# Kernel optimization log

Measured on AMD Instinct MI355X. Metric: run time of the kernel, lower is better.

Reference implementation:

```python
import jax, jax.numpy as jnp
import numpy as np

N, E, H, C = 20000, 320000, 4, 64
F_NODE, F_EDGE, F_W, T, LH = 64, 16, 8, 24, 64
NEG_SLOPE, EPS = 0.2, 1e-5


def setup_inputs() -> dict:
    key = jax.random.key(0)
    ks = jax.random.split(key, 20)
    d = {
        'node_static_features': jax.random.normal(ks[0], (N, F_NODE), jnp.float32),
        'edge_static_features': jax.random.normal(ks[1], (E, F_EDGE), jnp.float32),
        'node_dynamic_features': jax.random.normal(ks[2], (N, T, F_W), jnp.float32),
        'edge_index': jax.random.randint(ks[3], (E, 2), 0, N, jnp.int64),
        # GATConv params (PyG layout): shared lin for src/dst, lin_edge, att vectors, bias
        'W_lin': jax.random.normal(ks[4], (F_NODE, H * C), jnp.float32) / np.sqrt(F_NODE),
        'W_edge': jax.random.normal(ks[5], (F_EDGE, H * C), jnp.float32) / np.sqrt(F_EDGE),
        'att_src': jax.random.normal(ks[6], (H, C), jnp.float32) / np.sqrt(C),
        'att_dst': jax.random.normal(ks[7], (H, C), jnp.float32) / np.sqrt(C),
        'att_edge': jax.random.normal(ks[8], (H, C), jnp.float32) / np.sqrt(C),
        'gat_bias': jnp.zeros((C,), jnp.float32),
        # BatchNorm
        'bn_gamma': jnp.ones((C,), jnp.float32),
        'bn_beta': jnp.zeros((C,), jnp.float32),
        # LSTM (torch gate order i,f,g,o)
        'W_ih': jax.random.normal(ks[9], (4 * LH, F_W), jnp.float32) / np.sqrt(F_W),
        'W_hh': jax.random.normal(ks[10], (4 * LH, LH), jnp.float32) / np.sqrt(LH),
        'b_ih': jnp.zeros((4 * LH,), jnp.float32),
        'b_hh': jnp.zeros((4 * LH,), jnp.float32),
        # MLP head
        'W_hid': jax.random.normal(ks[11], (C + LH, C // 2), jnp.float32) / np.sqrt(C + LH),
        'b_hid': jnp.zeros((C // 2,), jnp.float32),
        'W_out': jax.random.normal(ks[12], (C // 2, 1), jnp.float32) / np.sqrt(C // 2),
        'b_out': jnp.zeros((1,), jnp.float32),
    }
    return d


def _gat_forward(x, edge_attr, src, dst, W_lin, W_edge, att_src, att_dst, att_edge, gat_bias):
    # add self loops with edge_attr fill_value='mean' (per-target mean of incoming edge feats)
    deg = jax.ops.segment_sum(jnp.ones((src.shape[0],), x.dtype), dst, num_segments=N)
    mean_attr = jax.ops.segment_sum(edge_attr, dst, num_segments=N) / jnp.maximum(deg, 1.0)[:, None]
    loop = jnp.arange(N, dtype=src.dtype)
    src = jnp.concatenate([src, loop]); dst = jnp.concatenate([dst, loop])
    edge_attr = jnp.concatenate([edge_attr, mean_attr], axis=0)  # [E+N, F_EDGE]

    xh = (x @ W_lin).reshape(N, H, C)                              # [N,H,C]
    eh = (edge_attr @ W_edge).reshape(-1, H, C)                    # [E+N,H,C]
    a_src = jnp.einsum('nhc,hc->nh', xh, att_src)                  # [N,H]
    a_dst = jnp.einsum('nhc,hc->nh', xh, att_dst)
    a_edge = jnp.einsum('ehc,hc->eh', eh, att_edge)
    alpha = a_src[src] + a_dst[dst] + a_edge                       # [E+N,H]
    alpha = jax.nn.leaky_relu(alpha, NEG_SLOPE)
    # segment softmax over edges grouped by destination node
    amax = jax.ops.segment_max(alpha, dst, num_segments=N)
    amax = jnp.where(jnp.isfinite(amax), amax, 0.0)
    ex = jnp.exp(alpha - amax[dst])
    denom = jax.ops.segment_sum(ex, dst, num_segments=N)
    attn = ex / (denom[dst] + 1e-16)                               # [E+N,H]
    msg = xh[src] * attn[:, :, None]                               # [E+N,H,C]
    out = jax.ops.segment_sum(msg, dst, num_segments=N)            # [N,H,C]
    return out.mean(axis=1) + gat_bias                             # concat=False -> head mean


def _lstm_last(xs, W_ih, W_hh, b_ih, b_hh):
    # xs: [N, T, F_W]; returns h_T: [N, LH]
    def step(carry, x_t):
        h, c = carry
        g = x_t @ W_ih.T + b_ih + h @ W_hh.T + b_hh
        i, f, gg, o = jnp.split(g, 4, axis=-1)
        c = jax.nn.sigmoid(f) * c + jax.nn.sigmoid(i) * jnp.tanh(gg)
        h = jax.nn.sigmoid(o) * jnp.tanh(c)
        return (h, c), None
    h0 = jnp.zeros((xs.shape[0], LH), xs.dtype)
    (h, _), _ = jax.lax.scan(step, (h0, h0), jnp.swapaxes(xs, 0, 1))
    return h


def reference(node_static_features, edge_static_features, node_dynamic_features, edge_index,
              W_lin, W_edge, att_src, att_dst, att_edge, gat_bias,
              bn_gamma, bn_beta, W_ih, W_hh, b_ih, b_hh,
              W_hid, b_hid, W_out, b_out):
    src, dst = edge_index[:, 0], edge_index[:, 1]
    x1 = _gat_forward(node_static_features, edge_static_features, src, dst,
                      W_lin, W_edge, att_src, att_dst, att_edge, gat_bias)
    # BatchNorm1d (training-mode batch stats) + relu; dropout is identity at eval
    mu = x1.mean(axis=0)
    var = x1.var(axis=0)
    x1 = jax.nn.relu((x1 - mu) / jnp.sqrt(var + EPS) * bn_gamma + bn_beta)
    h_last = _lstm_last(node_dynamic_features, W_ih, W_hh, b_ih, b_hh)  # [N,LH]
    combined = jnp.concatenate([x1, h_last], axis=1)
    hidden = jax.nn.relu(combined @ W_hid + b_hid)
    return hidden @ W_out + b_out  # [N,1]
```

## Files before the change

### kernel.cpp

```cpp
#include <hip/hip_runtime.h>
#include <hip/hip_bf16.h>

constexpr int N_  = 20000;
constexpr int E_  = 320000;
constexpr int T_  = 24;
constexpr float NEG_ = 0.2f;
constexpr float EPS_ = 1e-5f;
constexpr int MAXD_ = 128;
constexpr int LNB_ = 8;

typedef __attribute__((ext_vector_type(8)))  short short8v;
typedef __attribute__((ext_vector_type(16))) float f32x16;

__device__ __forceinline__ int esrc(const int* __restrict__ p, int e, int f64) {
    return f64 ? p[4 * e] : p[2 * e];
}
__device__ __forceinline__ int edst(const int* __restrict__ p, int e, int f64) {
    return f64 ? p[4 * e + 2] : p[2 * e + 1];
}

__device__ __forceinline__ float sigf(float x) {
    return __builtin_amdgcn_rcpf(1.f + __expf(-x));
}
__device__ __forceinline__ float tanhfast(float x) {
    return 1.f - 2.f * __builtin_amdgcn_rcpf(1.f + __expf(2.f * x));
}

__device__ __forceinline__ short f2bf(float f) {
    union { float f; unsigned u; } v; v.f = f;
    unsigned r = v.u + 0x7FFFu + ((v.u >> 16) & 1u);
    return (short)(r >> 16);
}
__device__ __forceinline__ float bf2f(unsigned short u) {
    return __uint_as_float((unsigned)u << 16);
}

__global__ void k_detect(const int* __restrict__ idx, int* __restrict__ flag) {
    int v = idx[2 * threadIdx.x + 1];
    unsigned long long b = __ballot(v != 0);
    if (threadIdx.x == 0) flag[0] = (b == 0ULL) ? 1 : 0;
}

__global__ __launch_bounds__(256) void k_Pq(
    const float* __restrict__ W_edge, const float* __restrict__ att_edge,
    const float* __restrict__ att_src, const float* __restrict__ att_dst,
    const float* __restrict__ W_lin, float* __restrict__ P, float* __restrict__ Q) {
    int t = threadIdx.x;
    if (t < 64) {
        int k = t >> 2, h = t & 3;
        float s = 0.f;
        for (int c = 0; c < 64; ++c) s += W_edge[k * 256 + h * 64 + c] * att_edge[h * 64 + c];
        P[k * 4 + h] = s;
    }
    {
        int k = t >> 2, h = t & 3;
        float s = 0.f, d = 0.f;
        for (int c = 0; c < 64; ++c) {
            float w = W_lin[k * 256 + h * 64 + c];
            s += w * att_src[h * 64 + c];
            d += w * att_dst[h * 64 + c];
        }
        Q[k * 8 + h] = s;
        Q[k * 8 + 4 + h] = d;
    }
}

__global__ __launch_bounds__(256) void k_node(
    const float* __restrict__ x, const float* __restrict__ W_lin,
    const float* __restrict__ Q,
    unsigned short* __restrict__ xhb, float* __restrict__ asrc, float* __restrict__ adst) {
    __shared__ float xs[16][65];
    __shared__ float Qsh[64][8];
    int t = threadIdx.x;
    int nb = blockIdx.x * 16;
    for (int i = t; i < 16 * 64; i += 256) xs[i >> 6][i & 63] = x[(long)nb * 64 + i];
    for (int i = t; i < 64 * 8; i += 256) ((float*)Qsh)[i] = Q[i];
    __syncthreads();
    float acc[16];
#pragma unroll
    for (int m = 0; m < 16; ++m) acc[m] = 0.f;
    for (int k = 0; k < 64; ++k) {
        float w = W_lin[k * 256 + t];
#pragma unroll
        for (int m = 0; m < 16; ++m) acc[m] += xs[m][k] * w;
    }
#pragma unroll
    for (int m = 0; m < 16; ++m) xhb[(long)(nb + m) * 256 + t] = (unsigned short)f2bf(acc[m]);
    if (t < 128) {
        int m = t >> 3, q = t & 7;
        float s = 0.f;
        for (int k = 0; k < 64; ++k) s += xs[m][k] * Qsh[k][q];
        if (q < 4) asrc[(nb + m) * 4 + q] = s;
        else       adst[(nb + m) * 4 + (q - 4)] = s;
    }
}

__global__ __launch_bounds__(256) void k_e1(
    const int* __restrict__ idx, const int* __restrict__ flag,
    const float* __restrict__ ea, const float* __restrict__ P,
    float4* __restrict__ aebuf, int* __restrict__ degi) {
    __shared__ float Ps[256];
    int t = threadIdx.x;
    if (t < 64) Ps[t] = P[t];
    __syncthreads();
    int e = blockIdx.x * 256 + t;
    if (e >= E_) return;
    int f64 = flag[0];
    int d = edst(idx, e, f64);
    const float* ep = ea + (long)e * 16;
    float ae[4] = {0.f, 0.f, 0.f, 0.f};
#pragma unroll
    for (int k = 0; k < 16; ++k) {
        float v = ep[k];
#pragma unroll
        for (int h = 0; h < 4; ++h) ae[h] += v * Ps[k * 4 + h];
    }
    aebuf[e] = make_float4(ae[0], ae[1], ae[2], ae[3]);
    atomicAdd(&degi[d], 1);
}

__global__ __launch_bounds__(256) void k_scan(const int* __restrict__ degi,
                                              int* __restrict__ offs) {
    __shared__ int part[256];
    int t = threadIdx.x;
    int base = t * 80;
    int s = 0;
    for (int i = 0; i < 80; ++i) { int ix = base + i; if (ix < N_) s += degi[ix]; }
    part[t] = s;
    __syncthreads();
    for (int d = 1; d < 256; d <<= 1) {
        int v = (t >= d) ? part[t - d] : 0;
        __syncthreads();
        part[t] += v;
        __syncthreads();
    }
    int run = (t > 0) ? part[t - 1] : 0;
    for (int i = 0; i < 80; ++i) {
        int ix = base + i;
        if (ix < N_) { offs[ix] = run; run += degi[ix]; }
    }
}

__global__ __launch_bounds__(256) void k_e2(
    const int* __restrict__ idx, const int* __restrict__ flag,
    const int* __restrict__ offs, int* __restrict__ cursor,
    int2* __restrict__ csr) {
    int e = blockIdx.x * 256 + threadIdx.x;
    if (e >= E_) return;
    int f64 = flag[0];
    int d = edst(idx, e, f64);
    int s = esrc(idx, e, f64);
    int pos = atomicAdd(&cursor[d], 1);
    csr[offs[d] + pos] = make_int2(e, s);
}

__global__ __launch_bounds__(256) void k_n2(
    const int* __restrict__ offs, const int* __restrict__ degi,
    const int2* __restrict__ csr, const float4* __restrict__ aebuf,
    const float4* __restrict__ asrc4, const float4* __restrict__ adst4,
    const unsigned short* __restrict__ xhb, const float* __restrict__ gat_bias,
    float* __restrict__ x1) {
    __shared__ int   sS[4][MAXD_];
    __shared__ float4 sEx[4][MAXD_];
    int t = threadIdx.x, w = t >> 6, lane = t & 63;
    int n = blockIdx.x * 4 + w;
    if (n >= N_) return;
    int deg = degi[n], off = offs[n];
    float4 ad = adst4[n];

    float4 aesum = make_float4(0, 0, 0, 0), den = make_float4(0, 0, 0, 0);
    for (int base = 0; base < deg; base += 64) {
        int i = base + lane;
        if (i < deg) {
            int2 pr = csr[off + i];
            float4 ae = aebuf[pr.x];
            float4 as = asrc4[pr.y];
            float a0 = as.x + ad.x + ae.x; a0 = a0 > 0.f ? a0 : NEG_ * a0;
            float a1 = as.y + ad.y + ae.y; a1 = a1 > 0.f ? a1 : NEG_ * a1;
            float a2 = as.z + ad.z + ae.z; a2 = a2 > 0.f ? a2 : NEG_ * a2;
            float a3 = as.w + ad.w + ae.w; a3 = a3 > 0.f ? a3 : NEG_ * a3;
            float4 ex = make_float4(__expf(a0), __expf(a1), __expf(a2), __expf(a3));
            aesum.x += ae.x; aesum.y += ae.y; aesum.z += ae.z; aesum.w += ae.w;
            den.x += ex.x; den.y += ex.y; den.z += ex.z; den.w += ex.w;
            if (i < MAXD_) { sS[w][i] = pr.y; sEx[w][i] = ex; }
        }
    }
#pragma unroll
    for (int m = 32; m >= 1; m >>= 1) {
        aesum.x += __shfl_xor(aesum.x, m); aesum.y += __shfl_xor(aesum.y, m);
        aesum.z += __shfl_xor(aesum.z, m); aesum.w += __shfl_xor(aesum.w, m);
        den.x += __shfl_xor(den.x, m); den.y += __shfl_xor(den.y, m);
        den.z += __shfl_xor(den.z, m); den.w += __shfl_xor(den.w, m);
    }
    float dv = fmaxf((float)deg, 1.f);
    float4 as = asrc4[n];
    float a0 = as.x + ad.x + aesum.x / dv; a0 = a0 > 0.f ? a0 : NEG_ * a0;
    float a1 = as.y + ad.y + aesum.y / dv; a1 = a1 > 0.f ? a1 : NEG_ * a1;
    float a2 = as.z + ad.z + aesum.z / dv; a2 = a2 > 0.f ? a2 : NEG_ * a2;
    float a3 = as.w + ad.w + aesum.w / dv; a3 = a3 > 0.f ? a3 : NEG_ * a3;
    float4 exs = make_float4(__expf(a0), __expf(a1), __expf(a2), __expf(a3));
    den.x += exs.x; den.y += exs.y; den.z += exs.z; den.w += exs.w;
    float i0 = 1.f / (den.x + 1e-16f), i1 = 1.f / (den.y + 1e-16f);
    float i2 = 1.f / (den.z + 1e-16f), i3 = 1.f / (den.w + 1e-16f);
    __syncthreads();

    float acc = 0.f;
#pragma unroll 2
    for (int i = 0; i < deg; ++i) {
        int s; float4 ex;
        if (i < MAXD_) { s = sS[w][i]; ex = sEx[w][i]; }
        else {
            int2 pr = csr[off + i];
            s = pr.y;
            float4 ae = aebuf[pr.x];
            float4 a5 = asrc4[s];
            float b0 = a5.x + ad.x + ae.x; b0 = b0 > 0.f ? b0 : NEG_ * b0;
            float b1 = a5.y + ad.y + ae.y; b1 = b1 > 0.f ? b1 : NEG_ * b1;
            float b2 = a5.z + ad.z + ae.z; b2 = b2 > 0.f ? b2 : NEG_ * b2;
            float b3 = a5.w + ad.w + ae.w; b3 = b3 > 0.f ? b3 : NEG_ * b3;
            ex = make_float4(__expf(b0), __expf(b1), __expf(b2), __expf(b3));
        }
        const unsigned short* xp = xhb + (long)s * 256;
        acc += ex.x * i0 * bf2f(xp[lane]) + ex.y * i1 * bf2f(xp[64 + lane])
             + ex.z * i2 * bf2f(xp[128 + lane]) + ex.w * i3 * bf2f(xp[192 + lane]);
    }
    {
        const unsigned short* xp = xhb + (long)n * 256;
        acc += exs.x * i0 * bf2f(xp[lane]) + exs.y * i1 * bf2f(xp[64 + lane])
             + exs.z * i2 * bf2f(xp[128 + lane]) + exs.w * i3 * bf2f(xp[192 + lane]);
    }
    x1[(long)n * 64 + lane] = acc * 0.25f + gat_bias[lane];
}

__global__ __launch_bounds__(256) void k_x1stats(
    const float* __restrict__ x1, float* __restrict__ bnsum) {
    int c = threadIdx.x & 63, r = threadIdx.x >> 6;
    float s = 0.f, s2 = 0.f;
    for (int n = blockIdx.x * 4 + r; n < N_; n += gridDim.x * 4) {
        float v = x1[(long)n * 64 + c];
        s += v; s2 += v * v;
    }
    __shared__ float red[4][128];
    red[r][c] = s; red[r][64 + c] = s2;
    __syncthreads();
    if (r == 0) {
        float ts = red[0][c] + red[1][c] + red[2][c] + red[3][c];
        float t2 = red[0][64 + c] + red[1][64 + c] + red[2][64 + c] + red[3][64 + c];
        atomicAdd(&bnsum[c], ts);
        atomicAdd(&bnsum[64 + c], t2);
    }
}

__global__ void k_bnfin(const float* __restrict__ bnsum, const float* __restrict__ gamma,
                        const float* __restrict__ beta, float* __restrict__ bnp) {
    int c = threadIdx.x;
    float mu = bnsum[c] / (float)N_;
    float var = bnsum[64 + c] / (float)N_ - mu * mu;
    float sc = gamma[c] * rsqrtf(var + EPS_);
    bnp[c] = sc;
    bnp[64 + c] = beta[c] - mu * sc;
}

__global__ __launch_bounds__(256, 2) void k_lstm_mfma(
    const float* __restrict__ xdyn, const float* __restrict__ W_ih,
    const float* __restrict__ W_hh, const float* __restrict__ b_ih,
    const float* __restrict__ b_hh, float* __restrict__ hlast) {
    __shared__ char lds[57344];
    char* W2b = lds + 32768;
    int t = threadIdx.x;
    int w = t >> 6, l = t & 63;
    int lm = l & 31, g = l >> 5;

    for (int idx = t; idx < 2048; idx += 256) {
        int ll = idx & 63, ks = (idx >> 6) & 3, t8 = idx >> 8;
        int j = 32 * t8 + (ll & 31);
        const float* wp = W_hh + j * 64 + 16 * ks + 8 * (ll >> 5);
        float4 wa = *(const float4*)wp;
        float4 wb = *(const float4*)(wp + 4);
        short8v f;
        f[0] = f2bf(wa.x); f[1] = f2bf(wa.y); f[2] = f2bf(wa.z); f[3] = f2bf(wa.w);
        f[4] = f2bf(wb.x); f[5] = f2bf(wb.y); f[6] = f2bf(wb.z); f[7] = f2bf(wb.w);
        *(short8v*)(lds + idx * 16) = f;
    }
    for (int idx = t; idx < 512; idx += 256) {
        int ll = idx & 63, t8 = idx >> 6;
        int j = 32 * t8 + (ll & 31);
        short8v f;
        if (ll < 32) {
            const float* wp = W_ih + j * 8;
            float4 wa = *(const float4*)wp;
            float4 wb = *(const float4*)(wp + 4);
            f[0] = f2bf(wa.x); f[1] = f2bf(wa.y); f[2] = f2bf(wa.z); f[3] = f2bf(wa.w);
            f[4] = f2bf(wb.x); f[5] = f2bf(wb.y); f[6] = f2bf(wb.z); f[7] = f2bf(wb.w);
        } else {
#pragma unroll
            for (int e = 0; e < 8; ++e) f[e] = 0;
            f[0] = f2bf(b_ih[j] + b_hh[j]);
        }
        *(short8v*)(W2b + idx * 16) = f;
    }
    char* Hb = lds + 40960 + w * 4096;
    {
        short8v zv;
#pragma unroll
        for (int e = 0; e < 8; ++e) zv[e] = 0;
#pragma unroll
        for (int i = l; i < 256; i += 64) ((short8v*)Hb)[i] = zv;
    }
    __syncthreads();

    const int nbase = blockIdx.x * 32 + w * LNB_;
    f32x16 zc;
#pragma unroll
    for (int e = 0; e < 16; ++e) zc[e] = 0.f;
    short8v xAc;
#pragma unroll
    for (int e = 0; e < 8; ++e) xAc[e] = 0;
    xAc[0] = (short)0x3F80;
    float cst[2][4];
#pragma unroll
    for (int jt = 0; jt < 2; ++jt)
#pragma unroll
        for (int r = 0; r < 4; ++r) cst[jt][r] = 0.f;

    const bool xld = (g == 0) && (lm < LNB_);
    const float* xbase = xdyn + (long)(nbase + (lm & (LNB_ - 1))) * T_ * 8;
    float4 xp0 = make_float4(0, 0, 0, 0), xp1 = make_float4(0, 0, 0, 0);
    if (xld) { xp0 = *(const float4*)xbase; xp1 = *(const float4*)(xbase + 4); }

    for (int t_ = 0; t_ < T_; ++t_) {
        short8v xA;
        if (g == 0) {
            if (xld) {
                xA[0] = f2bf(xp0.x); xA[1] = f2bf(xp0.y); xA[2] = f2bf(xp0.z); xA[3] = f2bf(xp0.w);
                xA[4] = f2bf(xp1.x); xA[5] = f2bf(xp1.y); xA[6] = f2bf(xp1.z); xA[7] = f2bf(xp1.w);
                if (t_ < T_ - 1) {
                    xp0 = *(const float4*)(xbase + (t_ + 1) * 8);
                    xp1 = *(const float4*)(xbase + (t_ + 1) * 8 + 4);
                }
            } else {
#pragma unroll
                for (int e = 0; e < 8; ++e) xA[e] = 0;
            }
        } else xA = xAc;

        short8v hA[4];
#pragma unroll
        for (int ks = 0; ks < 4; ++ks) {
            int raddr = (lm * 128 + 32 * ks + 16 * g) ^ ((lm & 7) << 4);
            hA[ks] = *(const short8v*)(Hb + raddr);
        }

        f32x16 acc[8];
#pragma unroll
        for (int t8 = 0; t8 < 8; ++t8) {
            short8v b2f = *(const short8v*)(W2b + (t8 * 64 + l) * 16);
            acc[t8] = __builtin_amdgcn_mfma_f32_32x32x16_bf16(xA, b2f, zc, 0, 0, 0);
        }
#pragma unroll
        for (int ks = 0; ks < 4; ++ks)
#pragma unroll
            for (int t8 = 0; t8 < 8; ++t8) {
                short8v bh = *(const short8v*)(lds + ((t8 * 4 + ks) * 64 + l) * 16);
                acc[t8] = __builtin_amdgcn_mfma_f32_32x32x16_bf16(hA[ks], bh, acc[t8], 0, 0, 0);
            }

#pragma unroll
        for (int jt = 0; jt < 2; ++jt) {
#pragma unroll
            for (int r = 0; r < 4; ++r) {
                float iv = acc[jt][r];
                float fv = acc[2 + jt][r];
                float gv = acc[4 + jt][r];
                float ov = acc[6 + jt][r];
                float si = sigf(iv), sf = sigf(fv), tg = tanhfast(gv), so = sigf(ov);
                float cn = sf * cst[jt][r] + si * tg;
                cst[jt][r] = cn;
                float hn = so * tanhfast(cn);
                int mrow = r + 4 * g;
                int j = 32 * jt + lm;
                int waddr = (mrow * 128 + j * 2) ^ ((mrow & 7) << 4);
                *(short*)(Hb + waddr) = f2bf(hn);
                if (t_ == T_ - 1) hlast[(long)(nbase + mrow) * 64 + j] = hn;
            }
        }
    }
}

__global__ __launch_bounds__(256) void k_head(
    const float* __restrict__ x1, const float* __restrict__ hlast,
    const float* __restrict__ bnp, const float* __restrict__ W_hid,
    const float* __restrict__ b_hid, const float* __restrict__ W_out,
    const float* __restrict__ b_out, float* __restrict__ out) {
    int n = blockIdx.x * 256 + threadIdx.x;
    if (n >= N_) return;
    float comb[128];
#pragma unroll
    for (int i = 0; i < 64; ++i)
        comb[i] = fmaxf(x1[(long)n * 64 + i] * bnp[i] + bnp[64 + i], 0.f);
#pragma unroll
    for (int i = 0; i < 64; ++i) comb[64 + i] = hlast[(long)n * 64 + i];
    float o = b_out[0];
    for (int j = 0; j < 32; ++j) {
        float a = b_hid[j];
#pragma unroll
        for (int i = 0; i < 128; ++i) a += comb[i] * W_hid[i * 32 + j];
        o += fmaxf(a, 0.f) * W_out[j];
    }
    out[n] = o;
}

extern "C" void kernel_launch(void* const* d_in, const int* in_sizes, int n_in,
                              void* d_out, int out_size, void* d_ws, size_t ws_size,
                              hipStream_t stream) {
    const float* x_node   = (const float*)d_in[0];
    const float* ea       = (const float*)d_in[1];
    const float* xdyn     = (const float*)d_in[2];
    const int*   eidx     = (const int*)d_in[3];
    const float* W_lin    = (const float*)d_in[4];
    const float* W_edge   = (const float*)d_in[5];
    const float* att_src  = (const float*)d_in[6];
    const float* att_dst  = (const float*)d_in[7];
    const float* att_edge = (const float*)d_in[8];
    const float* gat_bias = (const float*)d_in[9];
    const float* bn_gamma = (const float*)d_in[10];
    const float* bn_beta  = (const float*)d_in[11];
    const float* W_ih     = (const float*)d_in[12];
    const float* W_hh     = (const float*)d_in[13];
    const float* b_ih     = (const float*)d_in[14];
    const float* b_hh     = (const float*)d_in[15];
    const float* W_hid    = (const float*)d_in[16];
    const float* b_hid    = (const float*)d_in[17];
    const float* W_out    = (const float*)d_in[18];
    const float* b_out    = (const float*)d_in[19];
    float* out = (float*)d_out;

    char* ws = (char*)d_ws;
    size_t off = 0;
    auto alloc = [&](size_t bytes) -> void* {
        void* p = ws + off;
        off = (off + bytes + 255) & ~(size_t)255;
        return p;
    };
    int*      flag  = (int*)alloc(4);
    float*    P     = (float*)alloc(256 * 4);
    float*    Q     = (float*)alloc(64 * 8 * 4);
    float*    bnp   = (float*)alloc(128 * 4);
    char*     zs    = ws + off;
    float*    bnsum = (float*)alloc(128 * 4);
    int*      degi  = (int*)alloc((size_t)N_ * 4);
    int*      cursor= (int*)alloc((size_t)N_ * 4);
    size_t zbytes = (size_t)((ws + off) - zs);
    int*      offs  = (int*)alloc((size_t)N_ * 4);
    float4*   aebuf = (float4*)alloc((size_t)E_ * 16);
    int2*     csr   = (int2*)alloc((size_t)E_ * 8);
    unsigned short* xhb = (unsigned short*)alloc((size_t)N_ * 256 * 2);
    float*    asrc  = (float*)alloc((size_t)N_ * 4 * 4);
    float*    adst  = (float*)alloc((size_t)N_ * 4 * 4);
    float*    x1    = (float*)alloc((size_t)N_ * 64 * 4);
    float*    hlast = (float*)alloc((size_t)N_ * 64 * 4);
    (void)ws_size; (void)in_sizes; (void)n_in; (void)out_size;

    hipMemsetAsync(zs, 0, zbytes, stream);
    k_detect<<<1, 64, 0, stream>>>(eidx, flag);
    k_Pq<<<1, 256, 0, stream>>>(W_edge, att_edge, att_src, att_dst, W_lin, P, Q);
    k_node<<<N_ / 16, 256, 0, stream>>>(x_node, W_lin, Q, xhb, asrc, adst);
    k_e1<<<(E_ + 255) / 256, 256, 0, stream>>>(eidx, flag, ea, P, aebuf, degi);
    k_scan<<<1, 256, 0, stream>>>(degi, offs);
    k_e2<<<(E_ + 255) / 256, 256, 0, stream>>>(eidx, flag, offs, cursor, csr);
    k_n2<<<(N_ + 3) / 4, 256, 0, stream>>>(offs, degi, csr, aebuf,
                                           (const float4*)asrc, (const float4*)adst,
                                           xhb, gat_bias, x1);
    k_x1stats<<<128, 256, 0, stream>>>(x1, bnsum);
    k_bnfin<<<1, 64, 0, stream>>>(bnsum, bn_gamma, bn_beta, bnp);
    k_lstm_mfma<<<N_ / 32, 256, 0, stream>>>(xdyn, W_ih, W_hh, b_ih, b_hh, hlast);
    k_head<<<(N_ + 255) / 256, 256, 0, stream>>>(x1, hlast, bnp, W_hid, b_hid, W_out, b_out, out);
}
```

Measured before the change: 413.4 us.

## Merge setup kernels, LDS-stage scan, and hold half of LSTM W_hh in registers

Merges the index-format detect kernel and the P/Q precompute into one two-block launch. Also merges the node projection and per-edge attention/degree kernels into one launch using block-index ranges. The single-block scan now stages degrees in shared memory instead of reading global memory twice. The LSTM kernel keeps the first half of the bf16 W_hh fragments in registers, which cuts its LDS footprint and LDS traffic per step but raises register pressure, possibly hurting occupancy under launch_bounds(256,2).

```diff
diff --git a/kernel.cpp b/kernel.cpp
--- a/kernel.cpp
+++ b/kernel.cpp
@@ -35,17 +35,20 @@
     return __uint_as_float((unsigned)u << 16);
 }
 
-__global__ void k_detect(const int* __restrict__ idx, int* __restrict__ flag) {
-    int v = idx[2 * threadIdx.x + 1];
-    unsigned long long b = __ballot(v != 0);
-    if (threadIdx.x == 0) flag[0] = (b == 0ULL) ? 1 : 0;
-}
-
-__global__ __launch_bounds__(256) void k_Pq(
+__global__ __launch_bounds__(256) void k_init(
+    const int* __restrict__ idx, int* __restrict__ flag,
     const float* __restrict__ W_edge, const float* __restrict__ att_edge,
     const float* __restrict__ att_src, const float* __restrict__ att_dst,
     const float* __restrict__ W_lin, float* __restrict__ P, float* __restrict__ Q) {
     int t = threadIdx.x;
+    if (blockIdx.x == 0) {
+        if (t < 64) {
+            int v = idx[2 * t + 1];
+            unsigned long long b = __ballot(v != 0);
+            if (t == 0) flag[0] = (b == 0ULL) ? 1 : 0;
+        }
+        return;
+    }
     if (t < 64) {
         int k = t >> 2, h = t & 3;
         float s = 0.f;
@@ -65,67 +68,73 @@
     }
 }
 
-__global__ __launch_bounds__(256) void k_node(
+__global__ __launch_bounds__(256) void k_node_e1(
     const float* __restrict__ x, const float* __restrict__ W_lin,
     const float* __restrict__ Q,
-    unsigned short* __restrict__ xhb, float* __restrict__ asrc, float* __restrict__ adst) {
+    unsigned short* __restrict__ xhb, float* __restrict__ asrc, float* __restrict__ adst,
+    const int* __restrict__ idx, const int* __restrict__ flag,
+    const float* __restrict__ ea, const float* __restrict__ P,
+    float4* __restrict__ aebuf, int* __restrict__ degi) {
     __shared__ float xs[16][65];
     __shared__ float Qsh[64][8];
     int t = threadIdx.x;
-    int nb = blockIdx.x * 16;
-    for (int i = t; i < 16 * 64; i += 256) xs[i >> 6][i & 63] = x[(long)nb * 64 + i];
-    for (int i = t; i < 64 * 8; i += 256) ((float*)Qsh)[i] = Q[i];
-    __syncthreads();
-    float acc[16];
-#pragma unroll
-    for (int m = 0; m < 16; ++m) acc[m] = 0.f;
-    for (int k = 0; k < 64; ++k) {
-        float w = W_lin[k * 256 + t];
-#pragma unroll
-        for (int m = 0; m < 16; ++m) acc[m] += xs[m][k] * w;
-    }
-#pragma unroll
-    for (int m = 0; m < 16; ++m) xhb[(long)(nb + m) * 256 + t] = (unsigned short)f2bf(acc[m]);
-    if (t < 128) {
-        int m = t >> 3, q = t & 7;
-        float s = 0.f;
-        for (int k = 0; k < 64; ++k) s += xs[m][k] * Qsh[k][q];
-        if (q < 4) asrc[(nb + m) * 4 + q] = s;
-        else       adst[(nb + m) * 4 + (q - 4)] = s;
-    }
-}
-
-__global__ __launch_bounds__(256) void k_e1(
-    const int* __restrict__ idx, const int* __restrict__ flag,
-    const float* __restrict__ ea, const float* __restrict__ P,
-    float4* __restrict__ aebuf, int* __restrict__ degi) {
-    __shared__ float Ps[256];
-    int t = threadIdx.x;
-    if (t < 64) Ps[t] = P[t];
-    __syncthreads();
-    int e = blockIdx.x * 256 + t;
-    if (e >= E_) return;
-    int f64 = flag[0];
-    int d = edst(idx, e, f64);
-    const float* ep = ea + (long)e * 16;
-    float ae[4] = {0.f, 0.f, 0.f, 0.f};
-#pragma unroll
-    for (int k = 0; k < 16; ++k) {
-        float v = ep[k];
-#pragma unroll
-        for (int h = 0; h < 4; ++h) ae[h] += v * Ps[k * 4 + h];
-    }
-    aebuf[e] = make_float4(ae[0], ae[1], ae[2], ae[3]);
-    atomicAdd(&degi[d], 1);
+    if (blockIdx.x < 1250) {
+        int nb = blockIdx.x * 16;
+        for (int i = t; i < 16 * 64; i += 256) xs[i >> 6][i & 63] = x[(long)nb * 64 + i];
+        for (int i = t; i < 64 * 8; i += 256) ((float*)Qsh)[i] = Q[i];
+        __syncthreads();
+        float acc[16];
+#pragma unroll
+        for (int m = 0; m < 16; ++m) acc[m] = 0.f;
+        for (int k = 0; k < 64; ++k) {
+            float w = W_lin[k * 256 + t];
+#pragma unroll
+            for (int m = 0; m < 16; ++m) acc[m] += xs[m][k] * w;
+        }
+#pragma unroll
+        for (int m = 0; m < 16; ++m) xhb[(long)(nb + m) * 256 + t] = (unsigned short)f2bf(acc[m]);
+        if (t < 128) {
+            int m = t >> 3, q = t & 7;
+            float s = 0.f;
+            for (int k = 0; k < 64; ++k) s += xs[m][k] * Qsh[k][q];
+            if (q < 4) asrc[(nb + m) * 4 + q] = s;
+            else       adst[(nb + m) * 4 + (q - 4)] = s;
+        }
+    } else {
+        float* Ps = (float*)xs;
+        if (t < 64) Ps[t] = P[t];
+        __syncthreads();
+        int e = (blockIdx.x - 1250) * 256 + t;
+        if (e >= E_) return;
+        int f64 = flag[0];
+        int d = edst(idx, e, f64);
+        const float* ep = ea + (long)e * 16;
+        float ae[4] = {0.f, 0.f, 0.f, 0.f};
+#pragma unroll
+        for (int k = 0; k < 16; ++k) {
+            float v = ep[k];
+#pragma unroll
+            for (int h = 0; h < 4; ++h) ae[h] += v * Ps[k * 4 + h];
+        }
+        aebuf[e] = make_float4(ae[0], ae[1], ae[2], ae[3]);
+        atomicAdd(&degi[d], 1);
+    }
 }
 
 __global__ __launch_bounds__(256) void k_scan(const int* __restrict__ degi,
                                               int* __restrict__ offs) {
+    __shared__ int buf[20000];
     __shared__ int part[256];
     int t = threadIdx.x;
-    int base = t * 80;
+    for (int i = t; i < N_; i += 256) buf[i] = degi[i];
+    __syncthreads();
+    const int CH = 79;
+    int base = t * CH;
     int s = 0;
-    for (int i = 0; i < 80; ++i) { int ix = base + i; if (ix < N_) s += degi[ix]; }
+    for (int i = 0; i < CH; ++i) {
+        int ix = base + i;
+        if (ix < N_) { int v = buf[ix]; buf[ix] = s; s += v; }
+    }
     part[t] = s;
     __syncthreads();
     for (int d = 1; d < 256; d <<= 1) {
@@ -134,11 +143,13 @@
         part[t] += v;
         __syncthreads();
     }
-    int run = (t > 0) ? part[t - 1] : 0;
-    for (int i = 0; i < 80; ++i) {
+    int pb = (t > 0) ? part[t - 1] : 0;
+    for (int i = 0; i < CH; ++i) {
         int ix = base + i;
-        if (ix < N_) { offs[ix] = run; run += degi[ix]; }
-    }
+        if (ix < N_) buf[ix] += pb;
+    }
+    __syncthreads();
+    for (int i = t; i < N_; i += 256) offs[i] = buf[i];
 }
 
 __global__ __launch_bounds__(256) void k_e2(
@@ -265,16 +276,16 @@
     const float* __restrict__ xdyn, const float* __restrict__ W_ih,
     const float* __restrict__ W_hh, const float* __restrict__ b_ih,
     const float* __restrict__ b_hh, float* __restrict__ hlast) {
-    __shared__ char lds[57344];
-    char* W2b = lds + 32768;
+    __shared__ char lds[40960];
+    char* W2b = lds + 16384;
     int t = threadIdx.x;
     int w = t >> 6, l = t & 63;
     int lm = l & 31, g = l >> 5;
 
-    for (int idx = t; idx < 2048; idx += 256) {
-        int ll = idx & 63, ks = (idx >> 6) & 3, t8 = idx >> 8;
+    for (int idx = t; idx < 1024; idx += 256) {
+        int ll = idx & 63, ks2 = (idx >> 6) & 1, t8 = idx >> 7;
         int j = 32 * t8 + (ll & 31);
-        const float* wp = W_hh + j * 64 + 16 * ks + 8 * (ll >> 5);
+        const float* wp = W_hh + j * 64 + 16 * (2 + ks2) + 8 * (ll >> 5);
         float4 wa = *(const float4*)wp;
         float4 wb = *(const float4*)(wp + 4);
         short8v f;
@@ -299,7 +310,21 @@
         }
         *(short8v*)(W2b + idx * 16) = f;
     }
-    char* Hb = lds + 40960 + w * 4096;
+    short8v Bhr[8][2];
+#pragma unroll
+    for (int t8 = 0; t8 < 8; ++t8)
+#pragma unroll
+        for (int ks = 0; ks < 2; ++ks) {
+            int j = 32 * t8 + lm;
+            const float* wp = W_hh + j * 64 + 16 * ks + 8 * g;
+            float4 wa = *(const float4*)wp;
+            float4 wb = *(const float4*)(wp + 4);
+            short8v f;
+            f[0] = f2bf(wa.x); f[1] = f2bf(wa.y); f[2] = f2bf(wa.z); f[3] = f2bf(wa.w);
+            f[4] = f2bf(wb.x); f[5] = f2bf(wb.y); f[6] = f2bf(wb.z); f[7] = f2bf(wb.w);
+            Bhr[t8][ks] = f;
+        }
+    char* Hb = lds + 24576 + w * 4096;
     {
         short8v zv;
 #pragma unroll
@@ -358,11 +383,16 @@
             acc[t8] = __builtin_amdgcn_mfma_f32_32x32x16_bf16(xA, b2f, zc, 0, 0, 0);
         }
 #pragma unroll
-        for (int ks = 0; ks < 4; ++ks)
+        for (int ks = 0; ks < 2; ++ks)
+#pragma unroll
+            for (int t8 = 0; t8 < 8; ++t8)
+                acc[t8] = __builtin_amdgcn_mfma_f32_32x32x16_bf16(hA[ks], Bhr[t8][ks], acc[t8], 0, 0, 0);
+#pragma unroll
+        for (int ks2 = 0; ks2 < 2; ++ks2)
 #pragma unroll
             for (int t8 = 0; t8 < 8; ++t8) {
-                short8v bh = *(const short8v*)(lds + ((t8 * 4 + ks) * 64 + l) * 16);
-                acc[t8] = __builtin_amdgcn_mfma_f32_32x32x16_bf16(hA[ks], bh, acc[t8], 0, 0, 0);
+                short8v bh = *(const short8v*)(lds + ((t8 * 2 + ks2) * 64 + l) * 16);
+                acc[t8] = __builtin_amdgcn_mfma_f32_32x32x16_bf16(hA[2 + ks2], bh, acc[t8], 0, 0, 0);
             }
 
 #pragma unroll
@@ -462,10 +492,9 @@
     (void)ws_size; (void)in_sizes; (void)n_in; (void)out_size;
 
     hipMemsetAsync(zs, 0, zbytes, stream);
-    k_detect<<<1, 64, 0, stream>>>(eidx, flag);
-    k_Pq<<<1, 256, 0, stream>>>(W_edge, att_edge, att_src, att_dst, W_lin, P, Q);
-    k_node<<<N_ / 16, 256, 0, stream>>>(x_node, W_lin, Q, xhb, asrc, adst);
-    k_e1<<<(E_ + 255) / 256, 256, 0, stream>>>(eidx, flag, ea, P, aebuf, degi);
+    k_init<<<2, 256, 0, stream>>>(eidx, flag, W_edge, att_edge, att_src, att_dst, W_lin, P, Q);
+    k_node_e1<<<1250 + (E_ + 255) / 256, 256, 0, stream>>>(
+        x_node, W_lin, Q, xhb, asrc, adst, eidx, flag, ea, P, aebuf, degi);
     k_scan<<<1, 256, 0, stream>>>(degi, offs);
     k_e2<<<(E_ + 255) / 256, 256, 0, stream>>>(eidx, flag, offs, cursor, csr);
     k_n2<<<(N_ + 3) / 4, 256, 0, stream>>>(offs, degi, csr, aebuf,
```

Measured after the change: 422.1 us. 2.1% more time.
